# Performance work log

Hardware: AMD Instinct MI355X
Metric: run time of the kernel (lower is better)

Reference implementation:

```python
import jax, jax.numpy as jnp
import numpy as np

N_HEADS = 8

def setup_inputs() -> dict:
    key = jax.random.key(0)
    k0, k1, k2, k3, k4 = jax.random.split(key, 5)
    B, S, D = 2, 2048, 1024
    scale = 0.02
    return {
        "x": jax.random.normal(k0, (B, S, D), dtype=jnp.float32),
        "Wk": jax.random.normal(k1, (D, D), dtype=jnp.float32) * scale,
        "Wv": jax.random.normal(k2, (D, D), dtype=jnp.float32) * scale,
        "Wself": jax.random.normal(k3, (D, D), dtype=jnp.float32) * scale,
        "Wout": jax.random.normal(k4, (D, D), dtype=jnp.float32) * scale,
    }

def reference(x, Wk, Wv, Wself, Wout):
    B, S, D = x.shape
    H = N_HEADS
    hd = D // H
    # torch Linear: y = x @ W.T (no bias)
    keys = (x @ Wk.T).reshape(B, S, H, hd).transpose(0, 2, 1, 3)  # [B,H,S,hd]
    vals = (x @ Wv.T).reshape(B, S, H, hd).transpose(0, 2, 1, 3)  # [B,H,S,hd]
    # energy = K K^T / sqrt(hd); weights = softmax(-energy) with causal mask
    neg_energy = -jnp.einsum("bhqd,bhkd->bhqk", keys, keys) / jnp.sqrt(
        jnp.asarray(hd, dtype=x.dtype))
    causal = jnp.tril(jnp.ones((S, S), dtype=bool))  # allowed positions
    neg_energy = jnp.where(causal, neg_energy, -jnp.inf)
    weights = jax.nn.softmax(neg_energy, axis=-1)  # [B,H,S,S]
    pairwise = jnp.einsum("bhqk,bhkd->bhqd", weights, vals)
    pairwise = pairwise.transpose(0, 2, 1, 3).reshape(B, S, D)
    self_force = x @ Wself.T
    return (pairwise + self_force) @ Wout.T
```

## Files before the change

### kernel.cpp

```cpp
#include <hip/hip_runtime.h>


typedef unsigned short u16;
typedef short s16x8 __attribute__((ext_vector_type(8)));
typedef short s16x4 __attribute__((ext_vector_type(4)));
typedef unsigned short u16x4 __attribute__((ext_vector_type(4)));
typedef float f32x4 __attribute__((ext_vector_type(4)));

#define DEV __device__ __forceinline__

DEV u16 f2bf(float f) {
    union { float f; unsigned u; } v; v.f = f;
    return (u16)((v.u + 0x7FFFu + ((v.u >> 16) & 1u)) >> 16);
}
DEV float bf2f(u16 h) {
    union { unsigned u; float f; } v; v.u = ((unsigned)h) << 16;
    return v.f;
}
DEV void gload16(const void* g, void* l) {
    __builtin_amdgcn_global_load_lds(
        (const __attribute__((address_space(1))) void*)g,
        (__attribute__((address_space(3))) void*)l, 16, 0, 0);
}

#define FULL_BARRIER()                          \
    do {                                        \
        __builtin_amdgcn_sched_barrier(0);      \
        __builtin_amdgcn_s_barrier();           \
        __builtin_amdgcn_sched_barrier(0);      \
    } while (0)

__global__ __launch_bounds__(256) void cast_all(
    const float* __restrict__ x, const float* __restrict__ wk,
    const float* __restrict__ wv, const float* __restrict__ wsf,
    const float* __restrict__ wo,
    u16* __restrict__ xb, u16* __restrict__ wkb, u16* __restrict__ wvb,
    u16* __restrict__ wsb, u16* __restrict__ wob) {
    int i = blockIdx.x * 256 + threadIdx.x;
    const int NX = (2 * 2048 * 1024) / 4;
    const int NW = (1024 * 1024) / 4;
    const float* src; u16* dst; int off;
    if (i < NX)              { src = x;   dst = xb;  off = i; }
    else if (i < NX + NW)    { src = wk;  dst = wkb; off = i - NX; }
    else if (i < NX + 2*NW)  { src = wv;  dst = wvb; off = i - NX - NW; }
    else if (i < NX + 3*NW)  { src = wsf; dst = wsb; off = i - NX - 2*NW; }
    else                     { src = wo;  dst = wob; off = i - NX - 3*NW; }
    float4 v = ((const float4*)src)[off];
    u16x4 o = { f2bf(v.x), f2bf(v.y), f2bf(v.z), f2bf(v.w) };
    ((u16x4*)dst)[off] = o;
}

template <int MODE, int BN>
__global__ __launch_bounds__(256) void gemm_nt(
    const u16* __restrict__ A, const u16* __restrict__ W0,
    const u16* __restrict__ W1, const u16* __restrict__ W2,
    u16* __restrict__ O0, u16* __restrict__ O1, u16* __restrict__ O2,
    float* __restrict__ Of) {
    constexpr int NJ = BN / 32;
    constexpr int BLOADS = (BN * 64) / 4096;
    __shared__ __align__(16) u16 As[2][128 * 32];
    __shared__ __align__(16) u16 Bs[2][BN * 32];
    const int tid = threadIdx.x, lane = tid & 63, wave = tid >> 6;
    const int wr = wave >> 1, wc = wave & 1;
    const int m0 = blockIdx.y * 128, n0 = blockIdx.x * BN;
    const u16* Bw = W0;
    if (MODE == 0) Bw = (blockIdx.z == 0) ? W0 : (blockIdx.z == 1) ? W1 : W2;

    f32x4 acc[4][NJ];
#pragma unroll
    for (int i = 0; i < 4; ++i)
#pragma unroll
        for (int j = 0; j < NJ; ++j) acc[i][j] = f32x4{0.f, 0.f, 0.f, 0.f};

    const int o1 = wave * 1024 + lane * 16;
    const int r1 = o1 >> 6, c1 = (o1 & 63) >> 1;
    const int o2 = o1 + 4096;
    const int r2 = o2 >> 6, c2 = (o2 & 63) >> 1;

    auto stage = [&](int k0, int buf) {
        gload16(A + ((size_t)(m0 + r1) << 10) + k0 + c1, (char*)As[buf] + wave * 1024);
        gload16(A + ((size_t)(m0 + r2) << 10) + k0 + c2, (char*)As[buf] + 4096 + wave * 1024);
        gload16(Bw + ((size_t)(n0 + r1) << 10) + k0 + c1, (char*)Bs[buf] + wave * 1024);
        if (BLOADS == 2)
            gload16(Bw + ((size_t)(n0 + r2) << 10) + k0 + c2, (char*)Bs[buf] + 4096 + wave * 1024);
    };

    stage(0, 0);
    for (int t = 0; t < 32; ++t) {
        const int cur = t & 1;
        if (t < 31) {
            stage((t + 1) << 5, cur ^ 1);
            if constexpr (BLOADS == 2)
                asm volatile("s_waitcnt vmcnt(4)" ::: "memory");
            else
                asm volatile("s_waitcnt vmcnt(3)" ::: "memory");
        } else {
            asm volatile("s_waitcnt vmcnt(0)" ::: "memory");
        }
        FULL_BARRIER();
        const int kb = (lane >> 4) << 3;
        s16x8 af[4], bfr[NJ];
#pragma unroll
        for (int i = 0; i < 4; ++i)
            af[i] = *(const s16x8*)&As[cur][(wr * 64 + i * 16 + (lane & 15)) * 32 + kb];
#pragma unroll
        for (int j = 0; j < NJ; ++j)
            bfr[j] = *(const s16x8*)&Bs[cur][(wc * (BN / 2) + j * 16 + (lane & 15)) * 32 + kb];
#pragma unroll
        for (int i = 0; i < 4; ++i)
#pragma unroll
            for (int j = 0; j < NJ; ++j)
                acc[i][j] = __builtin_amdgcn_mfma_f32_16x16x32_bf16(af[i], bfr[j], acc[i][j], 0, 0, 0);
        FULL_BARRIER();
    }

    const int mb0 = m0 + wr * 64, nb0 = n0 + wc * (BN / 2);
    if (MODE == 1) {
#pragma unroll
        for (int i = 0; i < 4; ++i)
#pragma unroll
            for (int j = 0; j < NJ; ++j) {
                int n = nb0 + j * 16 + (lane & 15);
                int mbase = mb0 + i * 16 + ((lane >> 4) << 2);
#pragma unroll
                for (int r = 0; r < 4; ++r)
                    Of[((size_t)(mbase + r) << 10) + n] = acc[i][j][r];
            }
    } else if (blockIdx.z == 1) {
#pragma unroll
        for (int i = 0; i < 4; ++i)
#pragma unroll
            for (int j = 0; j < NJ; ++j) {
                int n = nb0 + j * 16 + (lane & 15);
                int h = n >> 7, d = n & 127;
                int mbase = mb0 + i * 16 + ((lane >> 4) << 2);
                int b = mbase >> 11, s = mbase & 2047;
                u16x4 pk;
#pragma unroll
                for (int r = 0; r < 4; ++r) pk[r] = f2bf(acc[i][j][r]);
                *(u16x4*)(O1 + (((size_t)(b * 8 + h) << 7) + d) * 2048 + s) = pk;
            }
    } else {
        u16* dst = blockIdx.z ? O2 : O0;
#pragma unroll
        for (int i = 0; i < 4; ++i)
#pragma unroll
            for (int j = 0; j < NJ; ++j) {
                int n = nb0 + j * 16 + (lane & 15);
                int mbase = mb0 + i * 16 + ((lane >> 4) << 2);
#pragma unroll
                for (int r = 0; r < 4; ++r)
                    dst[((size_t)(mbase + r) << 10) + n] = f2bf(acc[i][j][r]);
            }
    }
}

__global__ __launch_bounds__(256) void attn_kernel(
    const u16* __restrict__ Kb, const u16* __restrict__ Vtb,
    const u16* __restrict__ Sb, u16* __restrict__ Tb) {
    __shared__ __align__(16) u16 Ks[2][64 * 128];
    __shared__ __align__(16) u16 Vs[2][128 * 64];
    const int tid = threadIdx.x, lane = tid & 63, wave = tid >> 6;
    const int qt = (blockIdx.y & 8) ? blockIdx.x : (31 - blockIdx.x);
    const int bh = blockIdx.y, b = bh >> 3, h = bh & 7;
    const int hi = lane >> 4, lo = lane & 15;
    const int qlocal = wave * 16 + lo;
    const int qrow = qt * 64 + qlocal;

    s16x8 qf[4];
    {
        const u16* qp = Kb + ((size_t)(b * 2048 + qrow) << 10) + h * 128 + (hi << 3);
#pragma unroll
        for (int c = 0; c < 4; ++c) qf[c] = *(const s16x8*)(qp + c * 32);
    }

    const u16* ksrcb[4];
    const u16* vsrcb[4];
    int ldst[4];
#pragma unroll
    for (int j = 0; j < 4; ++j) {
        int p = wave * 4096 + j * 1024 + lane * 16;
        ldst[j] = wave * 4096 + j * 1024;
        int rk = p >> 8, cbs = (p & 255) ^ ((rk & 7) << 4);
        ksrcb[j] = Kb + ((size_t)(b * 2048 + rk) << 10) + h * 128 + (cbs >> 1);
        int dv = p >> 7, kbs = (p & 127) ^ ((dv & 7) << 4);
        vsrcb[j] = Vtb + (((size_t)(bh * 128 + dv)) << 11) + (kbs >> 1);
    }

    auto stage = [&](int ks0, int buf) {
        char* kb = (char*)Ks[buf];
        char* vb = (char*)Vs[buf];
#pragma unroll
        for (int j = 0; j < 4; ++j) {
            gload16(ksrcb[j] + ((size_t)ks0 << 10), kb + ldst[j]);
            gload16(vsrcb[j] + ks0, vb + ldst[j]);
        }
    };

    f32x4 oacc[8];
#pragma unroll
    for (int nf = 0; nf < 8; ++nf) oacc[nf] = f32x4{0.f, 0.f, 0.f, 0.f};
    float mrun = -__builtin_inff(), lrun = 0.f;
    const float SC = -0.12751741566723328f;

    stage(0, 0);
    asm volatile("s_waitcnt vmcnt(0)" ::: "memory");
    FULL_BARRIER();

    for (int kt = 0; kt <= qt; ++kt) {
        const int cur = kt & 1;
        if (kt < qt) {
            stage((kt + 1) << 6, cur ^ 1);
            asm volatile("s_waitcnt vmcnt(8)" ::: "memory");
        } else {
            asm volatile("s_waitcnt vmcnt(0)" ::: "memory");
        }
        FULL_BARRIER();

        f32x4 sf[4];
        __builtin_amdgcn_s_setprio(1);
#pragma unroll
        for (int mf = 0; mf < 4; ++mf) {
            f32x4 s = {0.f, 0.f, 0.f, 0.f};
            int kr = mf * 16 + lo;
            const char* rowp = (const char*)Ks[cur] + kr * 256;
            int swz = (kr & 7) << 4;
#pragma unroll
            for (int c = 0; c < 4; ++c) {
                s16x8 kf = *(const s16x8*)(rowp + ((c * 64 + hi * 16) ^ swz));
                s = __builtin_amdgcn_mfma_f32_16x16x32_bf16(kf, qf[c], s, 0, 0, 0);
            }
            sf[mf] = s;
        }
        __builtin_amdgcn_s_setprio(0);

        const bool diag = (kt == qt);
        float p[4][4];
        float pm = -__builtin_inff();
#pragma unroll
        for (int mf = 0; mf < 4; ++mf)
#pragma unroll
            for (int r = 0; r < 4; ++r) {
                float sv = sf[mf][r] * SC;
                if (diag) {
                    int klocal = mf * 16 + (hi << 2) + r;
                    if (klocal > qlocal) sv = -__builtin_inff();
                }
                p[mf][r] = sv;
                pm = fmaxf(pm, sv);
            }
        pm = fmaxf(pm, __shfl_xor(pm, 16));
        pm = fmaxf(pm, __shfl_xor(pm, 32));

        const bool grow = !__all(pm <= mrun);
        float mnew = grow ? fmaxf(mrun, pm) : mrun;
        if (grow) {
            float corr = exp2f(mrun - mnew);
            lrun *= corr;
            float cr[4];
#pragma unroll
            for (int r = 0; r < 4; ++r) cr[r] = __shfl(corr, (hi << 2) + r);
#pragma unroll
            for (int nf = 0; nf < 8; ++nf)
#pragma unroll
                for (int r = 0; r < 4; ++r) oacc[nf][r] *= cr[r];
            mrun = mnew;
        }

        float psum = 0.f;
        float p2[4][4];
#pragma unroll
        for (int mf = 0; mf < 4; ++mf)
#pragma unroll
            for (int r = 0; r < 4; ++r) {
                float e = exp2f(p[mf][r] - mnew);
                p2[mf][r] = e;
                psum += e;
            }
        psum += __shfl_xor(psum, 16);
        psum += __shfl_xor(psum, 32);
        lrun += psum;

        s16x8 pa[2];
#pragma unroll
        for (int c2 = 0; c2 < 2; ++c2) {
            s16x8 t;
#pragma unroll
            for (int e = 0; e < 4; ++e) t[e] = (short)f2bf(p2[2 * c2][e]);
#pragma unroll
            for (int e = 0; e < 4; ++e) t[4 + e] = (short)f2bf(p2[2 * c2 + 1][e]);
            pa[c2] = t;
        }
        __builtin_amdgcn_s_setprio(1);
#pragma unroll
        for (int nf = 0; nf < 8; ++nf) {
            int d = nf * 16 + lo;
            const char* vrow = (const char*)Vs[cur] + d * 128;
            int swz = (d & 7) << 4;
#pragma unroll
            for (int c2 = 0; c2 < 2; ++c2) {
                int ob = (hi << 3) + (c2 << 6);
                s16x4 vlo = *(const s16x4*)(vrow + (ob ^ swz));
                s16x4 vhi = *(const s16x4*)(vrow + ((ob + 32) ^ swz));
                s16x8 vf = {vlo[0], vlo[1], vlo[2], vlo[3], vhi[0], vhi[1], vhi[2], vhi[3]};
                oacc[nf] = __builtin_amdgcn_mfma_f32_16x16x32_bf16(pa[c2], vf, oacc[nf], 0, 0, 0);
            }
        }
        __builtin_amdgcn_s_setprio(0);

        FULL_BARRIER();
    }

    float linv[4];
#pragma unroll
    for (int r = 0; r < 4; ++r) linv[r] = 1.0f / __shfl(lrun, (hi << 2) + r);
#pragma unroll
    for (int nf = 0; nf < 8; ++nf) {
        int d = nf * 16 + lo;
#pragma unroll
        for (int r = 0; r < 4; ++r) {
            int q2 = qt * 64 + wave * 16 + (hi << 2) + r;
            size_t idx = ((size_t)(b * 2048 + q2) << 10) + h * 128 + d;
            Tb[idx] = f2bf(oacc[nf][r] * linv[r] + bf2f(Sb[idx]));
        }
    }
}

extern "C" void kernel_launch(void* const* d_in, const int* in_sizes, int n_in,
                              void* d_out, int out_size, void* d_ws, size_t ws_size,
                              hipStream_t stream) {
    const float* x   = (const float*)d_in[0];
    const float* Wk  = (const float*)d_in[1];
    const float* Wv  = (const float*)d_in[2];
    const float* Wsf = (const float*)d_in[3];
    const float* Wo  = (const float*)d_in[4];
    float* out = (float*)d_out;
    char* ws = (char*)d_ws;
    u16* xb  = (u16*)(ws);
    u16* wkb = (u16*)(ws + (8u << 20));
    u16* wvb = (u16*)(ws + (10u << 20));
    u16* wsb = (u16*)(ws + (12u << 20));
    u16* wob = (u16*)(ws + (14u << 20));
    u16* Kb  = (u16*)(ws + (16u << 20));
    u16* Vtb = (u16*)(ws + (24u << 20));
    u16* Sbf = (u16*)(ws + (32u << 20));
    u16* Tb  = xb;

    cast_all<<<8192, 256, 0, stream>>>(x, Wk, Wv, Wsf, Wo, xb, wkb, wvb, wsb, wob);
    gemm_nt<0, 128><<<dim3(8, 32, 3), 256, 0, stream>>>(xb, wkb, wvb, wsb, Kb, Vtb, Sbf, nullptr);
    attn_kernel<<<dim3(32, 16), 256, 0, stream>>>(Kb, Vtb, Sbf, Tb);
    gemm_nt<1, 64><<<dim3(16, 32, 1), 256, 0, stream>>>(Tb, wob, nullptr, nullptr,
                                                        nullptr, nullptr, nullptr, out);
}
```

Measured before the change: 227.7 us.

## Split causal attention KV range across two blocks and add combine kernel

Attention now splits each query tile's causal key range into two halves processed by separate blocks with 32-key tiles, writing partial outputs plus running max and sum. A new combine kernel merges the partials with the self-force term. This doubles the grid to improve load balance and occupancy on the many-CU device, at the cost of extra partial-output traffic and a launch. The GEMM loop also changes to a single barrier per k-step with the prefetch issued after the wait. The new path runs only if the workspace is large enough.

```diff
diff --git a/kernel.cpp b/kernel.cpp
--- a/kernel.cpp
+++ b/kernel.cpp
@@ -5,6 +5,7 @@
 typedef short s16x8 __attribute__((ext_vector_type(8)));
 typedef short s16x4 __attribute__((ext_vector_type(4)));
 typedef unsigned short u16x4 __attribute__((ext_vector_type(4)));
+typedef unsigned short u16x8 __attribute__((ext_vector_type(8)));
 typedef float f32x4 __attribute__((ext_vector_type(4)));
 
 #define DEV __device__ __forceinline__
@@ -81,23 +82,16 @@
         gload16(A + ((size_t)(m0 + r1) << 10) + k0 + c1, (char*)As[buf] + wave * 1024);
         gload16(A + ((size_t)(m0 + r2) << 10) + k0 + c2, (char*)As[buf] + 4096 + wave * 1024);
         gload16(Bw + ((size_t)(n0 + r1) << 10) + k0 + c1, (char*)Bs[buf] + wave * 1024);
-        if (BLOADS == 2)
+        if constexpr (BLOADS == 2)
             gload16(Bw + ((size_t)(n0 + r2) << 10) + k0 + c2, (char*)Bs[buf] + 4096 + wave * 1024);
     };
 
     stage(0, 0);
     for (int t = 0; t < 32; ++t) {
         const int cur = t & 1;
-        if (t < 31) {
-            stage((t + 1) << 5, cur ^ 1);
-            if constexpr (BLOADS == 2)
-                asm volatile("s_waitcnt vmcnt(4)" ::: "memory");
-            else
-                asm volatile("s_waitcnt vmcnt(3)" ::: "memory");
-        } else {
-            asm volatile("s_waitcnt vmcnt(0)" ::: "memory");
-        }
+        asm volatile("s_waitcnt vmcnt(0)" ::: "memory");
         FULL_BARRIER();
+        if (t < 31) stage((t + 1) << 5, cur ^ 1);
         const int kb = (lane >> 4) << 3;
         s16x8 af[4], bfr[NJ];
 #pragma unroll
@@ -111,7 +105,6 @@
 #pragma unroll
             for (int j = 0; j < NJ; ++j)
                 acc[i][j] = __builtin_amdgcn_mfma_f32_16x16x32_bf16(af[i], bfr[j], acc[i][j], 0, 0, 0);
-        FULL_BARRIER();
     }
 
     const int mb0 = m0 + wr * 64, nb0 = n0 + wc * (BN / 2);
@@ -153,6 +146,196 @@
                     dst[((size_t)(mbase + r) << 10) + n] = f2bf(acc[i][j][r]);
             }
     }
+}
+
+#define MINIT (-30000.0f)
+#define MASKV (-60000.0f)
+__global__ __launch_bounds__(256, 4) void attn_split(
+    const u16* __restrict__ Kb, const u16* __restrict__ Vtb,
+    u16* __restrict__ Op0, u16* __restrict__ Op1,
+    float* __restrict__ Mp, float* __restrict__ Lp) {
+    __shared__ __align__(16) u16 Ks[2][32 * 128];
+    __shared__ __align__(16) u16 Vs[2][128 * 32];
+    const int tid = threadIdx.x, lane = tid & 63, wave = tid >> 6;
+    const int q_raw = blockIdx.x >> 1, half = blockIdx.x & 1;
+    const int bh = blockIdx.y, b = bh >> 3, h = bh & 7;
+    const int qt = ((bh >> 2) & 1) ? q_raw : (31 - q_raw);
+    const int hi = lane >> 4, lo = lane & 15;
+    const int qrow = qt * 64 + wave * 16 + lo;
+
+    s16x8 qf[4];
+    {
+        const u16* qp = Kb + ((size_t)(b * 2048 + qrow) << 10) + h * 128 + (hi << 3);
+#pragma unroll
+        for (int c = 0; c < 4; ++c) qf[c] = *(const s16x8*)(qp + c * 32);
+    }
+
+    const u16* ksrc[2];
+    const u16* vsrc[2];
+    int ldst[2];
+#pragma unroll
+    for (int jj = 0; jj < 2; ++jj) {
+        int p = wave * 2048 + jj * 1024 + lane * 16;
+        ldst[jj] = wave * 2048 + jj * 1024;
+        int rk = p >> 8, cbs = (p & 255) ^ ((rk & 7) << 4);
+        ksrc[jj] = Kb + ((size_t)(b * 2048 + rk) << 10) + h * 128 + (cbs >> 1);
+        int dv = p >> 6, kbs = (p & 63) ^ ((dv & 3) << 4);
+        vsrc[jj] = Vtb + (((size_t)(bh * 128 + dv)) << 11) + (kbs >> 1);
+    }
+    auto stage = [&](int ks0, int buf) {
+        char* kb = (char*)Ks[buf];
+        char* vb = (char*)Vs[buf];
+#pragma unroll
+        for (int jj = 0; jj < 2; ++jj) {
+            gload16(ksrc[jj] + ((size_t)ks0 << 10), kb + ldst[jj]);
+            gload16(vsrc[jj] + ks0, vb + ldst[jj]);
+        }
+    };
+
+    f32x4 oacc[8];
+#pragma unroll
+    for (int nf = 0; nf < 8; ++nf) oacc[nf] = f32x4{0.f, 0.f, 0.f, 0.f};
+    float mrun = MINIT, lrun = 0.f;
+    const float SC = -0.12751741566723328f;
+
+    const int j0 = half ? (qt + 1) : 0;
+    const int j1 = j0 + qt + 1;
+
+    stage(j0 << 5, 0);
+    for (int j = j0; j < j1; ++j) {
+        const int cur = (j - j0) & 1;
+        asm volatile("s_waitcnt vmcnt(0)" ::: "memory");
+        FULL_BARRIER();
+        if (j + 1 < j1) stage((j + 1) << 5, cur ^ 1);
+
+        f32x4 sf[2];
+        __builtin_amdgcn_s_setprio(1);
+#pragma unroll
+        for (int mf = 0; mf < 2; ++mf) {
+            f32x4 s = {0.f, 0.f, 0.f, 0.f};
+            int kr = mf * 16 + lo;
+            const char* rowp = (const char*)Ks[cur] + kr * 256;
+            int swz = (kr & 7) << 4;
+#pragma unroll
+            for (int c = 0; c < 4; ++c) {
+                s16x8 kf = *(const s16x8*)(rowp + ((c * 64 + hi * 16) ^ swz));
+                s = __builtin_amdgcn_mfma_f32_16x16x32_bf16(kf, qf[c], s, 0, 0, 0);
+            }
+            sf[mf] = s;
+        }
+        __builtin_amdgcn_s_setprio(0);
+
+        const bool diag = (j >= 2 * qt);
+        float p[2][4];
+        float pm = MASKV;
+#pragma unroll
+        for (int mf = 0; mf < 2; ++mf)
+#pragma unroll
+            for (int r = 0; r < 4; ++r) {
+                float sv = sf[mf][r] * SC;
+                if (diag) {
+                    int kg = j * 32 + mf * 16 + (hi << 2) + r;
+                    if (kg > qrow) sv = MASKV;
+                }
+                p[mf][r] = sv;
+                pm = fmaxf(pm, sv);
+            }
+        pm = fmaxf(pm, __shfl_xor(pm, 16));
+        pm = fmaxf(pm, __shfl_xor(pm, 32));
+
+        const bool grow = !__all(pm <= mrun);
+        float mnew = mrun;
+        if (grow) {
+            mnew = fmaxf(mrun, pm);
+            float corr = exp2f(mrun - mnew);
+            lrun *= corr;
+            float cr[4];
+#pragma unroll
+            for (int r = 0; r < 4; ++r) cr[r] = __shfl(corr, (hi << 2) + r);
+#pragma unroll
+            for (int nf = 0; nf < 8; ++nf)
+#pragma unroll
+                for (int r = 0; r < 4; ++r) oacc[nf][r] *= cr[r];
+            mrun = mnew;
+        }
+
+        float psum = 0.f;
+        float p2[2][4];
+#pragma unroll
+        for (int mf = 0; mf < 2; ++mf)
+#pragma unroll
+            for (int r = 0; r < 4; ++r) {
+                float e = exp2f(p[mf][r] - mnew);
+                p2[mf][r] = e;
+                psum += e;
+            }
+        psum += __shfl_xor(psum, 16);
+        psum += __shfl_xor(psum, 32);
+        lrun += psum;
+
+        s16x8 pa;
+#pragma unroll
+        for (int e = 0; e < 4; ++e) pa[e] = (short)f2bf(p2[0][e]);
+#pragma unroll
+        for (int e = 0; e < 4; ++e) pa[4 + e] = (short)f2bf(p2[1][e]);
+
+        __builtin_amdgcn_s_setprio(1);
+#pragma unroll
+        for (int nf = 0; nf < 8; ++nf) {
+            int d = nf * 16 + lo;
+            const char* vrow = (const char*)Vs[cur] + d * 64;
+            int swz = (d & 3) << 4;
+            int ob = hi << 3;
+            s16x4 vlo = *(const s16x4*)(vrow + (ob ^ swz));
+            s16x4 vhi = *(const s16x4*)(vrow + ((ob + 32) ^ swz));
+            s16x8 vf = {vlo[0], vlo[1], vlo[2], vlo[3], vhi[0], vhi[1], vhi[2], vhi[3]};
+            oacc[nf] = __builtin_amdgcn_mfma_f32_16x16x32_bf16(pa, vf, oacc[nf], 0, 0, 0);
+        }
+        __builtin_amdgcn_s_setprio(0);
+    }
+
+    if (hi == 0) {
+        int mi = (half * 16 + bh) * 2048 + qrow;
+        Mp[mi] = mrun;
+        Lp[mi] = lrun;
+    }
+    u16* Op = half ? Op1 : Op0;
+#pragma unroll
+    for (int nf = 0; nf < 8; ++nf) {
+        int d = nf * 16 + lo;
+#pragma unroll
+        for (int r = 0; r < 4; ++r) {
+            int q2 = qt * 64 + wave * 16 + (hi << 2) + r;
+            Op[((size_t)(b * 2048 + q2) << 10) + h * 128 + d] = f2bf(oacc[nf][r]);
+        }
+    }
+}
+
+__global__ __launch_bounds__(256) void attn_combine(
+    const u16* __restrict__ O0, const u16* __restrict__ O1,
+    const float* __restrict__ Mp, const float* __restrict__ Lp,
+    const u16* __restrict__ Sb, u16* __restrict__ Tb) {
+    int i = blockIdx.x * 256 + threadIdx.x;
+    int d0 = (i & 15) << 3;
+    int row = i >> 4;
+    int h = row & 7;
+    int bq = row >> 3;
+    int b = bq >> 11, q = bq & 2047;
+    int bh = b * 8 + h;
+    int mi0 = bh * 2048 + q, mi1 = (16 + bh) * 2048 + q;
+    float m0 = Mp[mi0], m1 = Mp[mi1], l0 = Lp[mi0], l1 = Lp[mi1];
+    float m = fmaxf(m0, m1);
+    float a0 = exp2f(m0 - m), a1 = exp2f(m1 - m);
+    float rd = 1.0f / (l0 * a0 + l1 * a1);
+    size_t base = ((size_t)bq << 10) + (h << 7) + d0;
+    s16x8 o0 = *(const s16x8*)(O0 + base);
+    s16x8 o1 = *(const s16x8*)(O1 + base);
+    s16x8 sf = *(const s16x8*)(Sb + base);
+    u16x8 out;
+#pragma unroll
+    for (int e = 0; e < 8; ++e)
+        out[e] = f2bf((bf2f((u16)o0[e]) * a0 + bf2f((u16)o1[e]) * a1) * rd + bf2f((u16)sf[e]));
+    *(u16x8*)(Tb + base) = out;
 }
 
 __global__ __launch_bounds__(256) void attn_kernel(
@@ -173,7 +356,6 @@
 #pragma unroll
         for (int c = 0; c < 4; ++c) qf[c] = *(const s16x8*)(qp + c * 32);
     }
-
     const u16* ksrcb[4];
     const u16* vsrcb[4];
     int ldst[4];
@@ -186,7 +368,6 @@
         int dv = p >> 7, kbs = (p & 127) ^ ((dv & 7) << 4);
         vsrcb[j] = Vtb + (((size_t)(bh * 128 + dv)) << 11) + (kbs >> 1);
     }
-
     auto stage = [&](int ks0, int buf) {
         char* kb = (char*)Ks[buf];
         char* vb = (char*)Vs[buf];
@@ -196,7 +377,6 @@
             gload16(vsrcb[j] + ks0, vb + ldst[j]);
         }
     };
-
     f32x4 oacc[8];
 #pragma unroll
     for (int nf = 0; nf < 8; ++nf) oacc[nf] = f32x4{0.f, 0.f, 0.f, 0.f};
@@ -206,7 +386,6 @@
     stage(0, 0);
     asm volatile("s_waitcnt vmcnt(0)" ::: "memory");
     FULL_BARRIER();
-
     for (int kt = 0; kt <= qt; ++kt) {
         const int cur = kt & 1;
         if (kt < qt) {
@@ -216,7 +395,6 @@
             asm volatile("s_waitcnt vmcnt(0)" ::: "memory");
         }
         FULL_BARRIER();
-
         f32x4 sf[4];
         __builtin_amdgcn_s_setprio(1);
 #pragma unroll
@@ -233,7 +411,6 @@
             sf[mf] = s;
         }
         __builtin_amdgcn_s_setprio(0);
-
         const bool diag = (kt == qt);
         float p[4][4];
         float pm = -__builtin_inff();
@@ -251,7 +428,6 @@
             }
         pm = fmaxf(pm, __shfl_xor(pm, 16));
         pm = fmaxf(pm, __shfl_xor(pm, 32));
-
         const bool grow = !__all(pm <= mrun);
         float mnew = grow ? fmaxf(mrun, pm) : mrun;
         if (grow) {
@@ -266,7 +442,6 @@
                 for (int r = 0; r < 4; ++r) oacc[nf][r] *= cr[r];
             mrun = mnew;
         }
-
         float psum = 0.f;
         float p2[4][4];
 #pragma unroll
@@ -280,7 +455,6 @@
         psum += __shfl_xor(psum, 16);
         psum += __shfl_xor(psum, 32);
         lrun += psum;
-
         s16x8 pa[2];
 #pragma unroll
         for (int c2 = 0; c2 < 2; ++c2) {
@@ -307,10 +481,8 @@
             }
         }
         __builtin_amdgcn_s_setprio(0);
-
         FULL_BARRIER();
     }
-
     float linv[4];
 #pragma unroll
     for (int r = 0; r < 4; ++r) linv[r] = 1.0f / __shfl(lrun, (hi << 2) + r);
@@ -340,15 +512,31 @@
     u16* wkb = (u16*)(ws + (8u << 20));
     u16* wvb = (u16*)(ws + (10u << 20));
     u16* wsb = (u16*)(ws + (12u << 20));
-    u16* wob = (u16*)(ws + (14u << 20));
     u16* Kb  = (u16*)(ws + (16u << 20));
     u16* Vtb = (u16*)(ws + (24u << 20));
     u16* Sbf = (u16*)(ws + (32u << 20));
     u16* Tb  = xb;
 
-    cast_all<<<8192, 256, 0, stream>>>(x, Wk, Wv, Wsf, Wo, xb, wkb, wvb, wsb, wob);
-    gemm_nt<0, 128><<<dim3(8, 32, 3), 256, 0, stream>>>(xb, wkb, wvb, wsb, Kb, Vtb, Sbf, nullptr);
-    attn_kernel<<<dim3(32, 16), 256, 0, stream>>>(Kb, Vtb, Sbf, Tb);
-    gemm_nt<1, 64><<<dim3(16, 32, 1), 256, 0, stream>>>(Tb, wob, nullptr, nullptr,
-                                                        nullptr, nullptr, nullptr, out);
-}
+    const bool split = ws_size >= ((size_t)43u << 20);
+
+    if (split) {
+        u16* wob   = (u16*)(ws + (40u << 20));
+        u16* Op0   = xb;
+        u16* Op1   = (u16*)(ws + (8u << 20));
+        float* Mp  = (float*)(ws + (42u << 20));
+        float* Lp  = (float*)(ws + (42u << 20) + (256u << 10));
+        cast_all<<<8192, 256, 0, stream>>>(x, Wk, Wv, Wsf, Wo, xb, wkb, wvb, wsb, wob);
+        gemm_nt<0, 128><<<dim3(8, 32, 3), 256, 0, stream>>>(xb, wkb, wvb, wsb, Kb, Vtb, Sbf, nullptr);
+        attn_split<<<dim3(64, 16), 256, 0, stream>>>(Kb, Vtb, Op0, Op1, Mp, Lp);
+        attn_combine<<<2048, 256, 0, stream>>>(Op0, Op1, Mp, Lp, Sbf, Tb);
+        gemm_nt<1, 64><<<dim3(16, 32, 1), 256, 0, stream>>>(Tb, wob, nullptr, nullptr,
+                                                            nullptr, nullptr, nullptr, out);
+    } else {
+        u16* wob = (u16*)(ws + (14u << 20));
+        cast_all<<<8192, 256, 0, stream>>>(x, Wk, Wv, Wsf, Wo, xb, wkb, wvb, wsb, wob);
+        gemm_nt<0, 128><<<dim3(8, 32, 3), 256, 0, stream>>>(xb, wkb, wvb, wsb, Kb, Vtb, Sbf, nullptr);
+        attn_kernel<<<dim3(32, 16), 256, 0, stream>>>(Kb, Vtb, Sbf, Tb);
+        gemm_nt<1, 64><<<dim3(16, 32, 1), 256, 0, stream>>>(Tb, wob, nullptr, nullptr,
+                                                            nullptr, nullptr, nullptr, out);
+    }
+}
```

Result: slower. 239.0 us (+5.0%).

## Split causal attention KV range across two blocks and triple-buffer GEMM loads

Applied to the files above, without the earlier changes.

The attention kernel now processes each query tile in two halves of the key range, with 32-row key tiles. A new combine kernel merges the two partial outputs using the stored running max and sum, then adds the self-force term. This doubles the grid and is meant to raise occupancy and balance causal work. It costs an extra launch and the partial outputs round-trip through memory in bf16. The GEMM switches to a three-stage LDS buffer, prefetching two tiles ahead and dropping one barrier per iteration. Softmax probabilities are packed to bf16 with a packed convert instruction.

```diff
diff --git a/kernel.cpp b/kernel.cpp
--- a/kernel.cpp
+++ b/kernel.cpp
@@ -5,6 +5,7 @@
 typedef short s16x8 __attribute__((ext_vector_type(8)));
 typedef short s16x4 __attribute__((ext_vector_type(4)));
 typedef unsigned short u16x4 __attribute__((ext_vector_type(4)));
+typedef unsigned short u16x8 __attribute__((ext_vector_type(8)));
 typedef float f32x4 __attribute__((ext_vector_type(4)));
 
 #define DEV __device__ __forceinline__
@@ -58,8 +59,8 @@
     float* __restrict__ Of) {
     constexpr int NJ = BN / 32;
     constexpr int BLOADS = (BN * 64) / 4096;
-    __shared__ __align__(16) u16 As[2][128 * 32];
-    __shared__ __align__(16) u16 Bs[2][BN * 32];
+    __shared__ __align__(16) u16 As[3][128 * 32];
+    __shared__ __align__(16) u16 Bs[3][BN * 32];
     const int tid = threadIdx.x, lane = tid & 63, wave = tid >> 6;
     const int wr = wave >> 1, wc = wave & 1;
     const int m0 = blockIdx.y * 128, n0 = blockIdx.x * BN;
@@ -78,18 +79,20 @@
     const int r2 = o2 >> 6, c2 = (o2 & 63) >> 1;
 
     auto stage = [&](int k0, int buf) {
-        gload16(A + ((size_t)(m0 + r1) << 10) + k0 + c1, (char*)As[buf] + wave * 1024);
-        gload16(A + ((size_t)(m0 + r2) << 10) + k0 + c2, (char*)As[buf] + 4096 + wave * 1024);
-        gload16(Bw + ((size_t)(n0 + r1) << 10) + k0 + c1, (char*)Bs[buf] + wave * 1024);
-        if (BLOADS == 2)
-            gload16(Bw + ((size_t)(n0 + r2) << 10) + k0 + c2, (char*)Bs[buf] + 4096 + wave * 1024);
+        char* ab = (char*)As + buf * 8192;
+        char* bb = (char*)Bs + buf * (BN * 64);
+        gload16(A + ((size_t)(m0 + r1) << 10) + k0 + c1, ab + wave * 1024);
+        gload16(A + ((size_t)(m0 + r2) << 10) + k0 + c2, ab + 4096 + wave * 1024);
+        gload16(Bw + ((size_t)(n0 + r1) << 10) + k0 + c1, bb + wave * 1024);
+        if constexpr (BLOADS == 2)
+            gload16(Bw + ((size_t)(n0 + r2) << 10) + k0 + c2, bb + 4096 + wave * 1024);
     };
 
     stage(0, 0);
+    stage(32, 1);
+    int cur = 0;
     for (int t = 0; t < 32; ++t) {
-        const int cur = t & 1;
         if (t < 31) {
-            stage((t + 1) << 5, cur ^ 1);
             if constexpr (BLOADS == 2)
                 asm volatile("s_waitcnt vmcnt(4)" ::: "memory");
             else
@@ -98,20 +101,26 @@
             asm volatile("s_waitcnt vmcnt(0)" ::: "memory");
         }
         FULL_BARRIER();
+        if (t + 2 < 32) {
+            int nb = cur + 2; if (nb >= 3) nb -= 3;
+            stage((t + 2) << 5, nb);
+        }
         const int kb = (lane >> 4) << 3;
+        const u16* Ac = As[0] + cur * 4096;
+        const u16* Bc = Bs[0] + cur * (BN * 32);
         s16x8 af[4], bfr[NJ];
 #pragma unroll
         for (int i = 0; i < 4; ++i)
-            af[i] = *(const s16x8*)&As[cur][(wr * 64 + i * 16 + (lane & 15)) * 32 + kb];
+            af[i] = *(const s16x8*)&Ac[(wr * 64 + i * 16 + (lane & 15)) * 32 + kb];
 #pragma unroll
         for (int j = 0; j < NJ; ++j)
-            bfr[j] = *(const s16x8*)&Bs[cur][(wc * (BN / 2) + j * 16 + (lane & 15)) * 32 + kb];
+            bfr[j] = *(const s16x8*)&Bc[(wc * (BN / 2) + j * 16 + (lane & 15)) * 32 + kb];
 #pragma unroll
         for (int i = 0; i < 4; ++i)
 #pragma unroll
             for (int j = 0; j < NJ; ++j)
                 acc[i][j] = __builtin_amdgcn_mfma_f32_16x16x32_bf16(af[i], bfr[j], acc[i][j], 0, 0, 0);
-        FULL_BARRIER();
+        ++cur; if (cur == 3) cur = 0;
     }
 
     const int mb0 = m0 + wr * 64, nb0 = n0 + wc * (BN / 2);
@@ -155,17 +164,20 @@
     }
 }
 
-__global__ __launch_bounds__(256) void attn_kernel(
+#define MINIT (-30000.0f)
+#define MASKV (-60000.0f)
+__global__ __launch_bounds__(256, 4) void attn_split(
     const u16* __restrict__ Kb, const u16* __restrict__ Vtb,
-    const u16* __restrict__ Sb, u16* __restrict__ Tb) {
-    __shared__ __align__(16) u16 Ks[2][64 * 128];
-    __shared__ __align__(16) u16 Vs[2][128 * 64];
+    u16* __restrict__ Op0, u16* __restrict__ Op1,
+    float* __restrict__ Mp, float* __restrict__ Lp) {
+    __shared__ __align__(16) u16 Ks[2][32 * 128];
+    __shared__ __align__(16) u16 Vs[2][128 * 32];
     const int tid = threadIdx.x, lane = tid & 63, wave = tid >> 6;
-    const int qt = (blockIdx.y & 8) ? blockIdx.x : (31 - blockIdx.x);
+    const int q_raw = blockIdx.x >> 1, half = blockIdx.x & 1;
     const int bh = blockIdx.y, b = bh >> 3, h = bh & 7;
+    const int qt = ((bh >> 2) & 1) ? q_raw : (31 - q_raw);
     const int hi = lane >> 4, lo = lane & 15;
-    const int qlocal = wave * 16 + lo;
-    const int qrow = qt * 64 + qlocal;
+    const int qrow = qt * 64 + wave * 16 + lo;
 
     s16x8 qf[4];
     {
@@ -174,53 +186,48 @@
         for (int c = 0; c < 4; ++c) qf[c] = *(const s16x8*)(qp + c * 32);
     }
 
-    const u16* ksrcb[4];
-    const u16* vsrcb[4];
-    int ldst[4];
-#pragma unroll
-    for (int j = 0; j < 4; ++j) {
-        int p = wave * 4096 + j * 1024 + lane * 16;
-        ldst[j] = wave * 4096 + j * 1024;
+    const u16* ksrc[2];
+    const u16* vsrc[2];
+    int ldst[2];
+#pragma unroll
+    for (int jj = 0; jj < 2; ++jj) {
+        int p = wave * 2048 + jj * 1024 + lane * 16;
+        ldst[jj] = wave * 2048 + jj * 1024;
         int rk = p >> 8, cbs = (p & 255) ^ ((rk & 7) << 4);
-        ksrcb[j] = Kb + ((size_t)(b * 2048 + rk) << 10) + h * 128 + (cbs >> 1);
-        int dv = p >> 7, kbs = (p & 127) ^ ((dv & 7) << 4);
-        vsrcb[j] = Vtb + (((size_t)(bh * 128 + dv)) << 11) + (kbs >> 1);
-    }
-
+        ksrc[jj] = Kb + ((size_t)(b * 2048 + rk) << 10) + h * 128 + (cbs >> 1);
+        int dv = p >> 6, kbs = (p & 63) ^ ((dv & 3) << 4);
+        vsrc[jj] = Vtb + (((size_t)(bh * 128 + dv)) << 11) + (kbs >> 1);
+    }
     auto stage = [&](int ks0, int buf) {
         char* kb = (char*)Ks[buf];
         char* vb = (char*)Vs[buf];
 #pragma unroll
-        for (int j = 0; j < 4; ++j) {
-            gload16(ksrcb[j] + ((size_t)ks0 << 10), kb + ldst[j]);
-            gload16(vsrcb[j] + ks0, vb + ldst[j]);
+        for (int jj = 0; jj < 2; ++jj) {
+            gload16(ksrc[jj] + ((size_t)ks0 << 10), kb + ldst[jj]);
+            gload16(vsrc[jj] + ks0, vb + ldst[jj]);
         }
     };
 
     f32x4 oacc[8];
 #pragma unroll
     for (int nf = 0; nf < 8; ++nf) oacc[nf] = f32x4{0.f, 0.f, 0.f, 0.f};
-    float mrun = -__builtin_inff(), lrun = 0.f;
+    float mrun = MINIT, lrun = 0.f;
     const float SC = -0.12751741566723328f;
 
-    stage(0, 0);
-    asm volatile("s_waitcnt vmcnt(0)" ::: "memory");
-    FULL_BARRIER();
-
-    for (int kt = 0; kt <= qt; ++kt) {
-        const int cur = kt & 1;
-        if (kt < qt) {
-            stage((kt + 1) << 6, cur ^ 1);
-            asm volatile("s_waitcnt vmcnt(8)" ::: "memory");
-        } else {
-            asm volatile("s_waitcnt vmcnt(0)" ::: "memory");
-        }
+    const int j0 = half ? (qt + 1) : 0;
+    const int j1 = j0 + qt + 1;
+
+    stage(j0 << 5, 0);
+    for (int j = j0; j < j1; ++j) {
+        const int cur = (j - j0) & 1;
+        asm volatile("s_waitcnt vmcnt(0)" ::: "memory");
         FULL_BARRIER();
-
-        f32x4 sf[4];
+        if (j + 1 < j1) stage((j + 1) << 5, cur ^ 1);
+
+        f32x4 sf[2];
         __builtin_amdgcn_s_setprio(1);
 #pragma unroll
-        for (int mf = 0; mf < 4; ++mf) {
+        for (int mf = 0; mf < 2; ++mf) {
             f32x4 s = {0.f, 0.f, 0.f, 0.f};
             int kr = mf * 16 + lo;
             const char* rowp = (const char*)Ks[cur] + kr * 256;
@@ -234,17 +241,17 @@
         }
         __builtin_amdgcn_s_setprio(0);
 
-        const bool diag = (kt == qt);
-        float p[4][4];
-        float pm = -__builtin_inff();
-#pragma unroll
-        for (int mf = 0; mf < 4; ++mf)
+        const bool diag = (j >= 2 * qt);
+        float p[2][4];
+        float pm = MASKV;
+#pragma unroll
+        for (int mf = 0; mf < 2; ++mf)
 #pragma unroll
             for (int r = 0; r < 4; ++r) {
                 float sv = sf[mf][r] * SC;
                 if (diag) {
-                    int klocal = mf * 16 + (hi << 2) + r;
-                    if (klocal > qlocal) sv = -__builtin_inff();
+                    int kg = j * 32 + mf * 16 + (hi << 2) + r;
+                    if (kg > qrow) sv = MASKV;
                 }
                 p[mf][r] = sv;
                 pm = fmaxf(pm, sv);
@@ -253,8 +260,9 @@
         pm = fmaxf(pm, __shfl_xor(pm, 32));
 
         const bool grow = !__all(pm <= mrun);
-        float mnew = grow ? fmaxf(mrun, pm) : mrun;
+        float mnew = mrun;
         if (grow) {
+            mnew = fmaxf(mrun, pm);
             float corr = exp2f(mrun - mnew);
             lrun *= corr;
             float cr[4];
@@ -268,9 +276,9 @@
         }
 
         float psum = 0.f;
-        float p2[4][4];
-#pragma unroll
-        for (int mf = 0; mf < 4; ++mf)
+        float p2[2][4];
+#pragma unroll
+        for (int mf = 0; mf < 2; ++mf)
 #pragma unroll
             for (int r = 0; r < 4; ++r) {
                 float e = exp2f(p[mf][r] - mnew);
@@ -281,49 +289,72 @@
         psum += __shfl_xor(psum, 32);
         lrun += psum;
 
-        s16x8 pa[2];
-#pragma unroll
-        for (int c2 = 0; c2 < 2; ++c2) {
-            s16x8 t;
-#pragma unroll
-            for (int e = 0; e < 4; ++e) t[e] = (short)f2bf(p2[2 * c2][e]);
-#pragma unroll
-            for (int e = 0; e < 4; ++e) t[4 + e] = (short)f2bf(p2[2 * c2 + 1][e]);
-            pa[c2] = t;
-        }
+        unsigned pw0, pw1, pw2, pw3;
+        asm("v_cvt_pk_bf16_f32 %0, %1, %2" : "=v"(pw0) : "v"(p2[0][0]), "v"(p2[0][1]));
+        asm("v_cvt_pk_bf16_f32 %0, %1, %2" : "=v"(pw1) : "v"(p2[0][2]), "v"(p2[0][3]));
+        asm("v_cvt_pk_bf16_f32 %0, %1, %2" : "=v"(pw2) : "v"(p2[1][0]), "v"(p2[1][1]));
+        asm("v_cvt_pk_bf16_f32 %0, %1, %2" : "=v"(pw3) : "v"(p2[1][2]), "v"(p2[1][3]));
+        union { unsigned w[4]; s16x8 v; } pau;
+        pau.w[0] = pw0; pau.w[1] = pw1; pau.w[2] = pw2; pau.w[3] = pw3;
+        s16x8 pa = pau.v;
+
         __builtin_amdgcn_s_setprio(1);
 #pragma unroll
         for (int nf = 0; nf < 8; ++nf) {
             int d = nf * 16 + lo;
-            const char* vrow = (const char*)Vs[cur] + d * 128;
-            int swz = (d & 7) << 4;
-#pragma unroll
-            for (int c2 = 0; c2 < 2; ++c2) {
-                int ob = (hi << 3) + (c2 << 6);
-                s16x4 vlo = *(const s16x4*)(vrow + (ob ^ swz));
-                s16x4 vhi = *(const s16x4*)(vrow + ((ob + 32) ^ swz));
-                s16x8 vf = {vlo[0], vlo[1], vlo[2], vlo[3], vhi[0], vhi[1], vhi[2], vhi[3]};
-                oacc[nf] = __builtin_amdgcn_mfma_f32_16x16x32_bf16(pa[c2], vf, oacc[nf], 0, 0, 0);
-            }
+            const char* vrow = (const char*)Vs[cur] + d * 64;
+            int swz = (d & 3) << 4;
+            int ob = hi << 3;
+            s16x4 vlo = *(const s16x4*)(vrow + (ob ^ swz));
+            s16x4 vhi = *(const s16x4*)(vrow + ((ob + 32) ^ swz));
+            s16x8 vf = {vlo[0], vlo[1], vlo[2], vlo[3], vhi[0], vhi[1], vhi[2], vhi[3]};
+            oacc[nf] = __builtin_amdgcn_mfma_f32_16x16x32_bf16(pa, vf, oacc[nf], 0, 0, 0);
         }
         __builtin_amdgcn_s_setprio(0);
-
-        FULL_BARRIER();
-    }
-
-    float linv[4];
-#pragma unroll
-    for (int r = 0; r < 4; ++r) linv[r] = 1.0f / __shfl(lrun, (hi << 2) + r);
+    }
+
+    if (hi == 0) {
+        int mi = (half * 16 + bh) * 2048 + qrow;
+        Mp[mi] = mrun;
+        Lp[mi] = lrun;
+    }
+    u16* Op = half ? Op1 : Op0;
 #pragma unroll
     for (int nf = 0; nf < 8; ++nf) {
         int d = nf * 16 + lo;
 #pragma unroll
         for (int r = 0; r < 4; ++r) {
             int q2 = qt * 64 + wave * 16 + (hi << 2) + r;
-            size_t idx = ((size_t)(b * 2048 + q2) << 10) + h * 128 + d;
-            Tb[idx] = f2bf(oacc[nf][r] * linv[r] + bf2f(Sb[idx]));
-        }
-    }
+            Op[((size_t)(b * 2048 + q2) << 10) + h * 128 + d] = f2bf(oacc[nf][r]);
+        }
+    }
+}
+
+__global__ __launch_bounds__(256) void attn_combine(
+    const u16* __restrict__ O0, const u16* __restrict__ O1,
+    const float* __restrict__ Mp, const float* __restrict__ Lp,
+    const u16* __restrict__ Sb, u16* __restrict__ Tb) {
+    int i = blockIdx.x * 256 + threadIdx.x;
+    int d0 = (i & 15) << 3;
+    int row = i >> 4;
+    int h = row & 7;
+    int bq = row >> 3;
+    int b = bq >> 11, q = bq & 2047;
+    int bh = b * 8 + h;
+    int mi0 = bh * 2048 + q, mi1 = (16 + bh) * 2048 + q;
+    float m0 = Mp[mi0], m1 = Mp[mi1], l0 = Lp[mi0], l1 = Lp[mi1];
+    float m = fmaxf(m0, m1);
+    float a0 = exp2f(m0 - m), a1 = exp2f(m1 - m);
+    float rd = 1.0f / (l0 * a0 + l1 * a1);
+    size_t base = ((size_t)bq << 10) + (h << 7) + d0;
+    s16x8 o0 = *(const s16x8*)(O0 + base);
+    s16x8 o1 = *(const s16x8*)(O1 + base);
+    s16x8 sf = *(const s16x8*)(Sb + base);
+    u16x8 out;
+#pragma unroll
+    for (int e = 0; e < 8; ++e)
+        out[e] = f2bf((bf2f((u16)o0[e]) * a0 + bf2f((u16)o1[e]) * a1) * rd + bf2f((u16)sf[e]));
+    *(u16x8*)(Tb + base) = out;
 }
 
 extern "C" void kernel_launch(void* const* d_in, const int* in_sizes, int n_in,
@@ -340,15 +371,21 @@
     u16* wkb = (u16*)(ws + (8u << 20));
     u16* wvb = (u16*)(ws + (10u << 20));
     u16* wsb = (u16*)(ws + (12u << 20));
-    u16* wob = (u16*)(ws + (14u << 20));
     u16* Kb  = (u16*)(ws + (16u << 20));
     u16* Vtb = (u16*)(ws + (24u << 20));
     u16* Sbf = (u16*)(ws + (32u << 20));
     u16* Tb  = xb;
 
+    u16* wob   = (u16*)(ws + (40u << 20));
+    u16* Op0   = xb;
+    u16* Op1   = (u16*)(ws + (8u << 20));
+    float* Mp  = (float*)(ws + (42u << 20));
+    float* Lp  = (float*)(ws + (42u << 20) + (256u << 10));
+
     cast_all<<<8192, 256, 0, stream>>>(x, Wk, Wv, Wsf, Wo, xb, wkb, wvb, wsb, wob);
     gemm_nt<0, 128><<<dim3(8, 32, 3), 256, 0, stream>>>(xb, wkb, wvb, wsb, Kb, Vtb, Sbf, nullptr);
-    attn_kernel<<<dim3(32, 16), 256, 0, stream>>>(Kb, Vtb, Sbf, Tb);
+    attn_split<<<dim3(64, 16), 256, 0, stream>>>(Kb, Vtb, Op0, Op1, Mp, Lp);
+    attn_combine<<<2048, 256, 0, stream>>>(Op0, Op1, Mp, Lp, Sbf, Tb);
     gemm_nt<1, 64><<<dim3(16, 32, 1), 256, 0, stream>>>(Tb, wob, nullptr, nullptr,
                                                         nullptr, nullptr, nullptr, out);
 }
```

Result: no change. 228.1 us (+0.2%).
